# Optimization experiments

Hardware: AMD Instinct MI355X
Metric: run time of the kernel (lower is better)

Reference implementation:

```python
import jax, jax.numpy as jnp
import numpy as np

B, LQ, LK = 8, 1024, 1024
H, HD = 8, 128            # n_head, hidden_dim (per-head)
HEAD_DIM, CHILD_DIM = 512, 512
D_MODEL = HEAD_DIM + CHILD_DIM
TEMP = float(np.sqrt(HD))
NEG = 100000000.0
EPS = 1e-5


def setup_inputs() -> dict:
    key = jax.random.key(0)
    ks = jax.random.split(key, 12)
    q = jax.random.normal(ks[0], (B, LQ, HEAD_DIM), jnp.float32)
    k = jax.random.normal(ks[1], (B, LK, CHILD_DIM), jnp.float32)
    v = jax.random.normal(ks[2], (B, LK, D_MODEL), jnp.float32)
    old_score = 0.1 * jax.random.normal(ks[3], (H * B, LQ, LK), jnp.float32)
    float_mask = (jax.random.uniform(ks[4], (B, LQ, LK)) > 0.2).astype(jnp.float32)
    # torch nn.Linear weights are [out_features, in_features]
    wq = jax.random.normal(ks[5], (H * HD, HEAD_DIM), jnp.float32) * np.sqrt(2.0 / (HEAD_DIM + HD))
    wk = jax.random.normal(ks[6], (H * HD, CHILD_DIM), jnp.float32) * np.sqrt(2.0 / (CHILD_DIM + HD))
    wv = jax.random.normal(ks[7], (H * HD, D_MODEL), jnp.float32) * np.sqrt(2.0 / (D_MODEL + HD))
    wfc = jax.random.normal(ks[8], (D_MODEL, H * HD), jnp.float32) * np.sqrt(2.0 / (D_MODEL + H * HD))
    bq = jnp.zeros((H * HD,), jnp.float32)
    bk = jnp.zeros((H * HD,), jnp.float32)
    bv = jnp.zeros((H * HD,), jnp.float32)
    bfc = jnp.zeros((D_MODEL,), jnp.float32)
    ln_g = jnp.ones((D_MODEL,), jnp.float32)
    ln_b = jnp.zeros((D_MODEL,), jnp.float32)
    return dict(q=q, k=k, v=v, old_score=old_score, float_mask=float_mask,
                wq=wq, bq=bq, wk=wk, bk=bk, wv=wv, bv=bv,
                wfc=wfc, bfc=bfc, ln_g=ln_g, ln_b=ln_b)


def reference(q, k, v, old_score, float_mask, wq, bq, wk, bk, wv, bv, wfc, bfc, ln_g, ln_b):
    b, lq, _ = q.shape
    lk = k.shape[1]
    residual = v
    qh = (q @ wq.T + bq).reshape(b, lq, H, HD)   # [b,lq,h,d]
    kh = (k @ wk.T + bk).reshape(b, lk, H, HD)
    vh = (v @ wv.T + bv).reshape(b, lk, H, HD)
    # raw_score laid out head-major to match torch's (n_head*B, Lq, Lk)
    raw = jnp.einsum('bqhd,bkhd->hbqk', qh, kh) + old_score.reshape(H, b, lq, lk)
    score = raw - NEG * (1.0 - float_mask)[None]          # broadcast over heads
    attn = jax.nn.softmax(score / TEMP, axis=-1)          # eval path
    out = jnp.einsum('hbqk,bkhd->bqhd', attn, vh).reshape(b, lq, H * HD)
    out = out @ wfc.T + bfc + residual                    # dropout=identity (eval)
    mean = jnp.mean(out, axis=-1, keepdims=True)
    var = jnp.mean(jnp.square(out - mean), axis=-1, keepdims=True)
    out = (out - mean) / jnp.sqrt(var + EPS) * ln_g + ln_b
    return out, raw.reshape(H * b, lq, lk)
```

## Files before the change

### kernel.cpp

```cpp
#include <hip/hip_runtime.h>

typedef unsigned short u16;
typedef __bf16 bf16x8 __attribute__((ext_vector_type(8)));
typedef float f32x4 __attribute__((ext_vector_type(4)));

#define MFMA16(a,b,c) __builtin_amdgcn_mfma_f32_16x16x32_bf16(a,b,c,0,0,0)

static __device__ __forceinline__ u16 f2bf(float f){
  unsigned u = __builtin_bit_cast(unsigned, f);
  u += 0x7fffu + ((u>>16)&1u);
  return (u16)(u>>16);
}
static __device__ __forceinline__ int swz256(int r,int c){ return r*256 + (c ^ ((r&7)<<4)); }
static __device__ __forceinline__ int swz128(int r,int c){ return r*128 + (c ^ ((r&7)<<4)); }

static __device__ __forceinline__ void gload16(const void* g, void* l){
  __builtin_amdgcn_global_load_lds(
      (const __attribute__((address_space(1))) unsigned int*)g,
      (__attribute__((address_space(3))) unsigned int*)l, 16, 0, 0);
}

__global__ void conv_f2b(const float* __restrict__ in, u16* __restrict__ out, int n4){
  int i = blockIdx.x*256 + threadIdx.x;
  if (i >= n4) return;
  float4 f = reinterpret_cast<const float4*>(in)[i];
  ushort4 o; o.x=f2bf(f.x); o.y=f2bf(f.y); o.z=f2bf(f.z); o.w=f2bf(f.w);
  reinterpret_cast<ushort4*>(out)[i] = o;
}

template<int MODE>
__global__ __launch_bounds__(256) void gemm_nt(const u16* __restrict__ A, const u16* __restrict__ Bw,
    const float* __restrict__ bias, const float* __restrict__ resid,
    u16* __restrict__ Cb, float* __restrict__ Cf, int M, int N, int K)
{
  __shared__ uint4 ldsv[2048];
  char* la = (char*)ldsv;
  char* lb = la + 16384;
  const int tid = threadIdx.x, lane = tid&63, w = tid>>6;
  const int l15 = lane&15, l4 = lane>>4;
  const int wm = w&1, wn = w>>1;
  const int mb = blockIdx.x, nb = blockIdx.y;
  const f32x4 zero4 = {0.f,0.f,0.f,0.f};
  f32x4 acc[4][4];
  #pragma unroll
  for (int i=0;i<4;++i)
    #pragma unroll
    for (int j=0;j<4;++j) acc[i][j] = zero4;

  for (int k0=0;k0<K;k0+=64){
    __syncthreads();
    #pragma unroll
    for (int it=0; it<4; ++it){
      int slot = it*256 + tid;
      int r = slot>>3, cg = (slot&7) ^ (r&7);
      gload16(A + (size_t)(mb*128+r)*K + k0 + cg*8, la + (it*256 + w*64)*16);
      gload16(Bw + (size_t)(nb*128+r)*K + k0 + cg*8, lb + (it*256 + w*64)*16);
    }
    __syncthreads();
    #pragma unroll
    for (int kk=0;kk<2;++kk){
      bf16x8 af[4], bfr[4];
      #pragma unroll
      for (int i=0;i<4;++i){
        af[i]  = *reinterpret_cast<const bf16x8*>(la + swz128(wm*64+i*16+l15, (kk*32+l4*8)*2));
        bfr[i] = *reinterpret_cast<const bf16x8*>(lb + swz128(wn*64+i*16+l15, (kk*32+l4*8)*2));
      }
      #pragma unroll
      for (int i=0;i<4;++i)
        #pragma unroll
        for (int j=0;j<4;++j)
          acc[i][j] = MFMA16(af[i], bfr[j], acc[i][j]);
    }
  }
  #pragma unroll
  for (int j=0;j<4;++j){
    int col = nb*128 + wn*64 + j*16 + l15;
    float bv = bias[col];
    #pragma unroll
    for (int i=0;i<4;++i){
      int row0 = mb*128 + wm*64 + i*16 + l4*4;
      if (MODE == 0){
        #pragma unroll
        for (int r=0;r<4;++r)
          Cb[(size_t)(row0+r)*N + col] = f2bf(acc[i][j][r] + bv);
      } else if (MODE == 1){
        int bb = row0 >> 10, kp = row0 & 1023;
        ushort4 o;
        o.x = f2bf(acc[i][j][0]+bv); o.y = f2bf(acc[i][j][1]+bv);
        o.z = f2bf(acc[i][j][2]+bv); o.w = f2bf(acc[i][j][3]+bv);
        *reinterpret_cast<ushort4*>(Cb + (size_t)(bb*1024+col)*1024 + kp) = o;
      } else {
        #pragma unroll
        for (int r=0;r<4;++r){
          size_t off = (size_t)(row0+r)*N + col;
          Cf[off] = acc[i][j][r] + bv + resid[off];
        }
      }
    }
  }
}

__global__ __launch_bounds__(256) void attn_fused(const u16* __restrict__ qh,
    const u16* __restrict__ kh, const u16* __restrict__ vt,
    const float* __restrict__ oldsc, const float* __restrict__ fmask,
    float* __restrict__ raw, u16* __restrict__ ao)
{
  __shared__ uint4 ldsv[2560];
  char* lk_ = (char*)ldsv;
  char* lv_ = lk_ + 16384;
  char* lp_ = lk_ + 32768;
  const int tid = threadIdx.x, lane = tid&63, w = tid>>6;
  const int l15 = lane&15, l4 = lane>>4;
  const int qb = blockIdx.x, b = blockIdx.y, h = blockIdx.z;
  const float invT = 0.088388347648318447f;
  const f32x4 zero4 = {0.f,0.f,0.f,0.f};

  bf16x8 qf[4];
  {
    const u16* qp = qh + (size_t)(b*1024 + qb*64 + w*16 + l15)*1024 + h*128 + l4*8;
    #pragma unroll
    for (int kk=0;kk<4;++kk)
      qf[kk] = __builtin_bit_cast(bf16x8, *reinterpret_cast<const uint4*>(qp + kk*32));
  }
  f32x4 oacc[8];
  #pragma unroll
  for (int i=0;i<8;++i) oacc[i] = zero4;
  float mr[4], lr[4];
  #pragma unroll
  for (int r=0;r<4;++r){ mr[r] = -3.0e38f; lr[r] = 0.f; }

  const int qglob = qb*64 + w*16 + l4*4;

  for (int kt=0; kt<16; ++kt){
    __syncthreads();
    #pragma unroll
    for (int it=0; it<4; ++it){
      int slot = it*256 + tid;
      { int rs = slot>>4, cs = slot&15;
        int cg = cs ^ (rs&7);
        int kv = (rs&15)*4 + (rs>>4);
        gload16(kh + (size_t)(b*1024 + kt*64 + kv)*1024 + h*128 + cg*8,
                lk_ + (it*256 + w*64)*16); }
      { int r = slot>>3, cg = (slot&7) ^ (r&7);
        gload16(vt + (size_t)(b*1024 + h*128 + r)*1024 + kt*64 + cg*8,
                lv_ + (it*256 + w*64)*16); }
    }
    size_t rbase = ((size_t)(h*8 + b)*1024 + qglob)*1024 + kt*64 + l15*4;
    size_t mbase = ((size_t)b*1024 + qglob)*1024 + kt*64 + l15*4;
    float4 o4[4], m4[4];
    #pragma unroll
    for (int r=0;r<4;++r){
      o4[r] = *reinterpret_cast<const float4*>(oldsc + rbase + (size_t)r*1024);
      m4[r] = *reinterpret_cast<const float4*>(fmask + mbase + (size_t)r*1024);
    }
    __syncthreads();
    f32x4 fs[4];
    #pragma unroll
    for (int fj=0;fj<4;++fj){
      f32x4 s = zero4;
      #pragma unroll
      for (int kk=0;kk<4;++kk){
        bf16x8 kf = *reinterpret_cast<const bf16x8*>(lk_ + swz256(fj*16+l15, (kk*32+l4*8)*2));
        s = MFMA16(qf[kk], kf, s);
      }
      fs[fj] = s;
    }
    float tm[4];
    #pragma unroll
    for (int r=0;r<4;++r){
      float4 rv;
      rv.x = fs[0][r] + o4[r].x; rv.y = fs[1][r] + o4[r].y;
      rv.z = fs[2][r] + o4[r].z; rv.w = fs[3][r] + o4[r].w;
      *reinterpret_cast<float4*>(raw + rbase + (size_t)r*1024) = rv;
      fs[0][r] = (rv.x - 1.0e8f*(1.0f - m4[r].x)) * invT;
      fs[1][r] = (rv.y - 1.0e8f*(1.0f - m4[r].y)) * invT;
      fs[2][r] = (rv.z - 1.0e8f*(1.0f - m4[r].z)) * invT;
      fs[3][r] = (rv.w - 1.0e8f*(1.0f - m4[r].w)) * invT;
      tm[r] = fmaxf(fmaxf(fs[0][r], fs[1][r]), fmaxf(fs[2][r], fs[3][r]));
    }
    #pragma unroll
    for (int o=1;o<16;o<<=1){
      #pragma unroll
      for (int r=0;r<4;++r) tm[r] = fmaxf(tm[r], __shfl_xor(tm[r], o));
    }
    #pragma unroll
    for (int r=0;r<4;++r){
      float mn  = fmaxf(mr[r], tm[r]);
      float esc = __expf(mr[r] - mn);
      mr[r] = mn;
      lr[r] *= esc;
      #pragma unroll
      for (int nf=0;nf<8;++nf) oacc[nf][r] *= esc;
      float px = __expf(fs[0][r] - mn), py = __expf(fs[1][r] - mn);
      float pz = __expf(fs[2][r] - mn), pw = __expf(fs[3][r] - mn);
      lr[r] += px + py + pz + pw;
      ushort4 o;
      o.x = f2bf(px); o.y = f2bf(py); o.z = f2bf(pz); o.w = f2bf(pw);
      int prow = w*16 + l4*4 + r;
      *reinterpret_cast<ushort4*>(lp_ + swz128(prow, l15*8)) = o;
    }
    #pragma unroll
    for (int kkv=0;kkv<2;++kkv){
      bf16x8 pf = *reinterpret_cast<const bf16x8*>(lp_ + swz128(w*16+l15, (kkv*32+l4*8)*2));
      #pragma unroll
      for (int nf=0;nf<8;++nf){
        bf16x8 vf = *reinterpret_cast<const bf16x8*>(lv_ + swz128(nf*16+l15, (kkv*32+l4*8)*2));
        oacc[nf] = MFMA16(pf, vf, oacc[nf]);
      }
    }
  }
  #pragma unroll
  for (int o=1;o<16;o<<=1){
    #pragma unroll
    for (int r=0;r<4;++r) lr[r] += __shfl_xor(lr[r], o);
  }
  #pragma unroll
  for (int nf=0;nf<8;++nf){
    int col = h*128 + nf*16 + l15;
    #pragma unroll
    for (int r=0;r<4;++r){
      size_t orow = (size_t)(b*1024 + qb*64 + w*16 + l4*4 + r);
      ao[orow*1024 + col] = f2bf(oacc[nf][r] * (1.0f/lr[r]));
    }
  }
}

__global__ __launch_bounds__(256) void ln_k(float* __restrict__ io,
    const float* __restrict__ g, const float* __restrict__ bb)
{
  const int lane = threadIdx.x & 63, w = threadIdx.x >> 6;
  size_t row = (size_t)blockIdx.x*4 + w;
  float4* p = reinterpret_cast<float4*>(io + row*1024);
  float4 x[4];
  float s = 0.f, s2 = 0.f;
  #pragma unroll
  for (int i=0;i<4;++i){
    x[i] = p[lane + i*64];
    s  += x[i].x + x[i].y + x[i].z + x[i].w;
    s2 += x[i].x*x[i].x + x[i].y*x[i].y + x[i].z*x[i].z + x[i].w*x[i].w;
  }
  #pragma unroll
  for (int o=1;o<64;o<<=1){ s += __shfl_xor(s,o); s2 += __shfl_xor(s2,o); }
  float mean = s * 0.0009765625f;
  float var  = s2 * 0.0009765625f - mean*mean;
  float rstd = rsqrtf(var + 1e-5f);
  const float4* gp = reinterpret_cast<const float4*>(g);
  const float4* bp = reinterpret_cast<const float4*>(bb);
  #pragma unroll
  for (int i=0;i<4;++i){
    float4 gg = gp[lane+i*64], bv = bp[lane+i*64], y;
    y.x = (x[i].x-mean)*rstd*gg.x + bv.x;
    y.y = (x[i].y-mean)*rstd*gg.y + bv.y;
    y.z = (x[i].z-mean)*rstd*gg.z + bv.z;
    y.w = (x[i].w-mean)*rstd*gg.w + bv.w;
    p[lane+i*64] = y;
  }
}

extern "C" void kernel_launch(void* const* d_in, const int* in_sizes, int n_in,
                              void* d_out, int out_size, void* d_ws, size_t ws_size,
                              hipStream_t stream)
{
  const float* q    = (const float*)d_in[0];
  const float* k    = (const float*)d_in[1];
  const float* v    = (const float*)d_in[2];
  const float* olds = (const float*)d_in[3];
  const float* fm   = (const float*)d_in[4];
  const float* wq   = (const float*)d_in[5];
  const float* bq   = (const float*)d_in[6];
  const float* wk   = (const float*)d_in[7];
  const float* bk   = (const float*)d_in[8];
  const float* wv   = (const float*)d_in[9];
  const float* bv   = (const float*)d_in[10];
  const float* wfc  = (const float*)d_in[11];
  const float* bfc  = (const float*)d_in[12];
  const float* lng  = (const float*)d_in[13];
  const float* lnb  = (const float*)d_in[14];
  float* out = (float*)d_out;
  float* raw = out + 8388608;

  u16* ws  = (u16*)d_ws;
  u16* qbf = ws;
  u16* kbf = qbf + 4194304;
  u16* vbf = kbf + 4194304;
  u16* wqb = vbf + 8388608;
  u16* wkb = wqb + 524288;
  u16* wvb = wkb + 524288;
  u16* wfb = wvb + 1048576;
  u16* qhb = wfb + 1048576;
  u16* khb = qhb + 8388608;
  u16* vtb = khb + 8388608;
  u16* aob = vtb + 8388608;

  conv_f2b<<<4096,256,0,stream>>>(q,   qbf, 1048576);
  conv_f2b<<<4096,256,0,stream>>>(k,   kbf, 1048576);
  conv_f2b<<<8192,256,0,stream>>>(v,   vbf, 2097152);
  conv_f2b<<<512, 256,0,stream>>>(wq,  wqb, 131072);
  conv_f2b<<<512, 256,0,stream>>>(wk,  wkb, 131072);
  conv_f2b<<<1024,256,0,stream>>>(wv,  wvb, 262144);
  conv_f2b<<<1024,256,0,stream>>>(wfc, wfb, 262144);

  gemm_nt<0><<<dim3(64,8),256,0,stream>>>(qbf, wqb, bq, nullptr, qhb, nullptr, 8192,1024,512);
  gemm_nt<0><<<dim3(64,8),256,0,stream>>>(kbf, wkb, bk, nullptr, khb, nullptr, 8192,1024,512);
  gemm_nt<1><<<dim3(64,8),256,0,stream>>>(vbf, wvb, bv, nullptr, vtb, nullptr, 8192,1024,1024);

  attn_fused<<<dim3(16,8,8),256,0,stream>>>(qhb, khb, vtb, olds, fm, raw, aob);

  gemm_nt<2><<<dim3(64,8),256,0,stream>>>(aob, wfb, bfc, v, nullptr, out, 8192,1024,1024);
  ln_k<<<2048,256,0,stream>>>(out, lng, lnb);
}
```

Measured before the change: 316.1 us.

## Double-buffer K/V tiles and prefetch old_score/mask in attention kernel

Splits the attention loop into stage, prefetch and compute steps and ping-pongs between two LDS buffers for the K and V tiles. The next tile's K/V global-to-LDS loads and old_score/mask register loads are issued before the current tile is computed, so memory latency can overlap the MFMA work and one barrier per iteration is removed. In exchange, LDS use per block nearly doubles, which lowers the number of resident blocks per CU. The barrier at the end of each body step may also force all outstanding loads to finish, which would limit how much overlap is actually achieved.

```diff
diff --git a/kernel.cpp b/kernel.cpp
--- a/kernel.cpp
+++ b/kernel.cpp
@@ -105,16 +105,25 @@
     const float* __restrict__ oldsc, const float* __restrict__ fmask,
     float* __restrict__ raw, u16* __restrict__ ao)
 {
-  __shared__ uint4 ldsv[2560];
-  char* lk_ = (char*)ldsv;
-  char* lv_ = lk_ + 16384;
-  char* lp_ = lk_ + 32768;
+  __shared__ uint4 ldsv[4608];
+  char* lk0 = (char*)ldsv;
+  char* lv0 = lk0 + 16384;
+  char* lk1 = lk0 + 32768;
+  char* lv1 = lk0 + 49152;
+  char* lp_ = lk0 + 65536;
   const int tid = threadIdx.x, lane = tid&63, w = tid>>6;
   const int l15 = lane&15, l4 = lane>>4;
   const int qb = blockIdx.x, b = blockIdx.y, h = blockIdx.z;
   const float invT = 0.088388347648318447f;
   const f32x4 zero4 = {0.f,0.f,0.f,0.f};
 
+  const int qglob = qb*64 + w*16 + l4*4;
+  const float* oldp = oldsc + ((size_t)(h*8+b)*1024 + qglob)*1024 + l15*4;
+  const float* fmp  = fmask + ((size_t)b*1024 + qglob)*1024 + l15*4;
+  float*       rawp = raw   + ((size_t)(h*8+b)*1024 + qglob)*1024 + l15*4;
+  const u16* khB = kh + (size_t)b*1024*1024 + h*128;
+  const u16* vtB = vt + ((size_t)b*1024 + h*128)*1024;
+
   bf16x8 qf[4];
   {
     const u16* qp = qh + (size_t)(b*1024 + qb*64 + w*16 + l15)*1024 + h*128 + l4*8;
@@ -129,38 +138,33 @@
   #pragma unroll
   for (int r=0;r<4;++r){ mr[r] = -3.0e38f; lr[r] = 0.f; }
 
-  const int qglob = qb*64 + w*16 + l4*4;
-
-  for (int kt=0; kt<16; ++kt){
-    __syncthreads();
+  auto stage = [&](int kt, char* lkD, char* lvD){
     #pragma unroll
     for (int it=0; it<4; ++it){
       int slot = it*256 + tid;
-      { int rs = slot>>4, cs = slot&15;
-        int cg = cs ^ (rs&7);
-        int kv = (rs&15)*4 + (rs>>4);
-        gload16(kh + (size_t)(b*1024 + kt*64 + kv)*1024 + h*128 + cg*8,
-                lk_ + (it*256 + w*64)*16); }
-      { int r = slot>>3, cg = (slot&7) ^ (r&7);
-        gload16(vt + (size_t)(b*1024 + h*128 + r)*1024 + kt*64 + cg*8,
-                lv_ + (it*256 + w*64)*16); }
-    }
-    size_t rbase = ((size_t)(h*8 + b)*1024 + qglob)*1024 + kt*64 + l15*4;
-    size_t mbase = ((size_t)b*1024 + qglob)*1024 + kt*64 + l15*4;
-    float4 o4[4], m4[4];
+      int rs = slot>>4, cs = slot&15;
+      int cgk = cs ^ (rs&7);
+      int kv = (rs&15)*4 + (rs>>4);
+      gload16(khB + (size_t)(kt*64 + kv)*1024 + cgk*8, lkD + (it*256 + w*64)*16);
+      int r8 = slot>>3, cgv = (slot&7) ^ (r8&7);
+      gload16(vtB + (size_t)r8*1024 + kt*64 + cgv*8, lvD + (it*256 + w*64)*16);
+    }
+  };
+  auto pref = [&](int kt, float4 (&o4)[4], float4 (&m4)[4]){
     #pragma unroll
     for (int r=0;r<4;++r){
-      o4[r] = *reinterpret_cast<const float4*>(oldsc + rbase + (size_t)r*1024);
-      m4[r] = *reinterpret_cast<const float4*>(fmask + mbase + (size_t)r*1024);
-    }
-    __syncthreads();
+      o4[r] = *reinterpret_cast<const float4*>(oldp + (size_t)r*1024 + kt*64);
+      m4[r] = *reinterpret_cast<const float4*>(fmp  + (size_t)r*1024 + kt*64);
+    }
+  };
+  auto body = [&](int kt, char* lkR, char* lvR, float4 (&o4)[4], float4 (&m4)[4]){
     f32x4 fs[4];
     #pragma unroll
     for (int fj=0;fj<4;++fj){
       f32x4 s = zero4;
       #pragma unroll
       for (int kk=0;kk<4;++kk){
-        bf16x8 kf = *reinterpret_cast<const bf16x8*>(lk_ + swz256(fj*16+l15, (kk*32+l4*8)*2));
+        bf16x8 kf = *reinterpret_cast<const bf16x8*>(lkR + swz256(fj*16+l15, (kk*32+l4*8)*2));
         s = MFMA16(qf[kk], kf, s);
       }
       fs[fj] = s;
@@ -171,7 +175,7 @@
       float4 rv;
       rv.x = fs[0][r] + o4[r].x; rv.y = fs[1][r] + o4[r].y;
       rv.z = fs[2][r] + o4[r].z; rv.w = fs[3][r] + o4[r].w;
-      *reinterpret_cast<float4*>(raw + rbase + (size_t)r*1024) = rv;
+      *reinterpret_cast<float4*>(rawp + (size_t)r*1024 + kt*64) = rv;
       fs[0][r] = (rv.x - 1.0e8f*(1.0f - m4[r].x)) * invT;
       fs[1][r] = (rv.y - 1.0e8f*(1.0f - m4[r].y)) * invT;
       fs[2][r] = (rv.z - 1.0e8f*(1.0f - m4[r].z)) * invT;
@@ -204,11 +208,25 @@
       bf16x8 pf = *reinterpret_cast<const bf16x8*>(lp_ + swz128(w*16+l15, (kkv*32+l4*8)*2));
       #pragma unroll
       for (int nf=0;nf<8;++nf){
-        bf16x8 vf = *reinterpret_cast<const bf16x8*>(lv_ + swz128(nf*16+l15, (kkv*32+l4*8)*2));
+        bf16x8 vf = *reinterpret_cast<const bf16x8*>(lvR + swz128(nf*16+l15, (kkv*32+l4*8)*2));
         oacc[nf] = MFMA16(pf, vf, oacc[nf]);
       }
     }
-  }
+    __syncthreads();
+  };
+
+  float4 oA[4], mA[4], oB[4], mB[4];
+  stage(0, lk0, lv0);
+  pref(0, oA, mA);
+  __syncthreads();
+  for (int kt=0; kt<16; kt+=2){
+    stage(kt+1, lk1, lv1);
+    pref(kt+1, oB, mB);
+    body(kt, lk0, lv0, oA, mA);
+    if (kt+2 < 16){ stage(kt+2, lk0, lv0); pref(kt+2, oA, mA); }
+    body(kt+1, lk1, lv1, oB, mB);
+  }
+
   #pragma unroll
   for (int o=1;o<16;o<<=1){
     #pragma unroll
```

New measurement: 313.2 us. About the same (-0.9%).

## Bitpack mask, widen attention KV tile, prefetch old_score, remap blocks to XCDs

Applied to the files above, without the earlier changes.

Packs the float mask into one bit per element in a pre-pass, so the attention kernel reads 1/32 of the mask bytes it read before. The attention kernel now uses 128-wide KV tiles (LDS doubled) and prefetches old_score and mask bits one tile ahead, with double-buffered registers and explicit waitcnt/barrier scheduling. It also remaps the 1D grid so that blocks sharing the same (b,h) K/V land on the same XCD for L2 reuse. The cost is an extra kernel launch plus more LDS and registers, which can lower occupancy.

```diff
diff --git a/kernel.cpp b/kernel.cpp
--- a/kernel.cpp
+++ b/kernel.cpp
@@ -26,6 +26,22 @@
   float4 f = reinterpret_cast<const float4*>(in)[i];
   ushort4 o; o.x=f2bf(f.x); o.y=f2bf(f.y); o.z=f2bf(f.z); o.w=f2bf(f.w);
   reinterpret_cast<ushort4*>(out)[i] = o;
+}
+
+__global__ void mask2bits(const float* __restrict__ fm, unsigned char* __restrict__ bits){
+  int i = blockIdx.x*256 + threadIdx.x;
+  const float4* p = reinterpret_cast<const float4*>(fm + (size_t)i*8);
+  float4 a = p[0], bq = p[1];
+  unsigned v = 0;
+  v |= (a.x  > 0.5f) ? 1u   : 0u;
+  v |= (a.y  > 0.5f) ? 2u   : 0u;
+  v |= (a.z  > 0.5f) ? 4u   : 0u;
+  v |= (a.w  > 0.5f) ? 8u   : 0u;
+  v |= (bq.x > 0.5f) ? 16u  : 0u;
+  v |= (bq.y > 0.5f) ? 32u  : 0u;
+  v |= (bq.z > 0.5f) ? 64u  : 0u;
+  v |= (bq.w > 0.5f) ? 128u : 0u;
+  bits[i] = (unsigned char)v;
 }
 
 template<int MODE>
@@ -102,18 +118,28 @@
 
 __global__ __launch_bounds__(256) void attn_fused(const u16* __restrict__ qh,
     const u16* __restrict__ kh, const u16* __restrict__ vt,
-    const float* __restrict__ oldsc, const float* __restrict__ fmask,
+    const float* __restrict__ oldsc, const unsigned char* __restrict__ bits,
     float* __restrict__ raw, u16* __restrict__ ao)
 {
-  __shared__ uint4 ldsv[2560];
+  __shared__ uint4 ldsv[5120];
   char* lk_ = (char*)ldsv;
-  char* lv_ = lk_ + 16384;
-  char* lp_ = lk_ + 32768;
+  char* lv_ = lk_ + 32768;
+  char* lp_ = lk_ + 65536;
   const int tid = threadIdx.x, lane = tid&63, w = tid>>6;
   const int l15 = lane&15, l4 = lane>>4;
-  const int qb = blockIdx.x, b = blockIdx.y, h = blockIdx.z;
+  unsigned u = blockIdx.x;
+  int slotid = (u & 7) * 128 + (u >> 3);
+  const int qb = slotid & 15, bh = slotid >> 4;
+  const int b = bh & 7, h = bh >> 3;
   const float invT = 0.088388347648318447f;
   const f32x4 zero4 = {0.f,0.f,0.f,0.f};
+
+  const int qglob = qb*64 + w*16 + l4*4;
+  const float* oldp = oldsc + ((size_t)(h*8+b)*1024 + qglob)*1024 + l15*8;
+  float*       rawp = raw   + ((size_t)(h*8+b)*1024 + qglob)*1024 + l15*8;
+  const unsigned char* bitp = bits + ((size_t)b*1024 + qglob)*128 + l15;
+  const u16* khB = kh + (size_t)b*1024*1024 + h*128;
+  const u16* vtB = vt + ((size_t)b*1024 + h*128)*1024;
 
   bf16x8 qf[4];
   {
@@ -129,34 +155,35 @@
   #pragma unroll
   for (int r=0;r<4;++r){ mr[r] = -3.0e38f; lr[r] = 0.f; }
 
-  const int qglob = qb*64 + w*16 + l4*4;
-
-  for (int kt=0; kt<16; ++kt){
-    __syncthreads();
-    #pragma unroll
-    for (int it=0; it<4; ++it){
+  auto stage = [&](int kt){
+    #pragma unroll
+    for (int it=0; it<8; ++it){
       int slot = it*256 + tid;
-      { int rs = slot>>4, cs = slot&15;
-        int cg = cs ^ (rs&7);
-        int kv = (rs&15)*4 + (rs>>4);
-        gload16(kh + (size_t)(b*1024 + kt*64 + kv)*1024 + h*128 + cg*8,
-                lk_ + (it*256 + w*64)*16); }
-      { int r = slot>>3, cg = (slot&7) ^ (r&7);
-        gload16(vt + (size_t)(b*1024 + h*128 + r)*1024 + kt*64 + cg*8,
-                lv_ + (it*256 + w*64)*16); }
-    }
-    size_t rbase = ((size_t)(h*8 + b)*1024 + qglob)*1024 + kt*64 + l15*4;
-    size_t mbase = ((size_t)b*1024 + qglob)*1024 + kt*64 + l15*4;
-    float4 o4[4], m4[4];
+      int rs = slot>>4, cs = slot&15;
+      int ck = cs ^ (rs&7);
+      int ks = (rs&15)*8 + (rs>>4);
+      gload16(khB + (size_t)(kt*128 + ks)*1024 + ck*8, lk_ + (it*256 + w*64)*16);
+    }
+    #pragma unroll
+    for (int it=0; it<8; ++it){
+      int slot = it*256 + tid;
+      int rs = slot>>4, cs = slot&15;
+      int cv = cs ^ (rs&7);
+      gload16(vtB + (size_t)rs*1024 + kt*128 + cv*8, lv_ + (it*256 + w*64)*16);
+    }
+  };
+  auto pref = [&](int kt, float4 (&o8)[4][2], unsigned (&bb)[4]){
     #pragma unroll
     for (int r=0;r<4;++r){
-      o4[r] = *reinterpret_cast<const float4*>(oldsc + rbase + (size_t)r*1024);
-      m4[r] = *reinterpret_cast<const float4*>(fmask + mbase + (size_t)r*1024);
-    }
-    __syncthreads();
-    f32x4 fs[4];
-    #pragma unroll
-    for (int fj=0;fj<4;++fj){
+      o8[r][0] = *reinterpret_cast<const float4*>(oldp + (size_t)r*1024 + kt*128);
+      o8[r][1] = *reinterpret_cast<const float4*>(oldp + (size_t)r*1024 + kt*128 + 4);
+      bb[r] = bitp[(size_t)r*128 + kt*16];
+    }
+  };
+  auto body = [&](int kt, float4 (&o8)[4][2], unsigned (&bb)[4]){
+    f32x4 fs[8];
+    #pragma unroll
+    for (int fj=0;fj<8;++fj){
       f32x4 s = zero4;
       #pragma unroll
       for (int kk=0;kk<4;++kk){
@@ -168,15 +195,25 @@
     float tm[4];
     #pragma unroll
     for (int r=0;r<4;++r){
-      float4 rv;
-      rv.x = fs[0][r] + o4[r].x; rv.y = fs[1][r] + o4[r].y;
-      rv.z = fs[2][r] + o4[r].z; rv.w = fs[3][r] + o4[r].w;
-      *reinterpret_cast<float4*>(raw + rbase + (size_t)r*1024) = rv;
-      fs[0][r] = (rv.x - 1.0e8f*(1.0f - m4[r].x)) * invT;
-      fs[1][r] = (rv.y - 1.0e8f*(1.0f - m4[r].y)) * invT;
-      fs[2][r] = (rv.z - 1.0e8f*(1.0f - m4[r].z)) * invT;
-      fs[3][r] = (rv.w - 1.0e8f*(1.0f - m4[r].w)) * invT;
-      tm[r] = fmaxf(fmaxf(fs[0][r], fs[1][r]), fmaxf(fs[2][r], fs[3][r]));
+      float4 r0, r1;
+      r0.x = fs[0][r] + o8[r][0].x; r0.y = fs[1][r] + o8[r][0].y;
+      r0.z = fs[2][r] + o8[r][0].z; r0.w = fs[3][r] + o8[r][0].w;
+      r1.x = fs[4][r] + o8[r][1].x; r1.y = fs[5][r] + o8[r][1].y;
+      r1.z = fs[6][r] + o8[r][1].z; r1.w = fs[7][r] + o8[r][1].w;
+      float4* rp = reinterpret_cast<float4*>(rawp + (size_t)r*1024 + kt*128);
+      rp[0] = r0; rp[1] = r1;
+      unsigned bv = bb[r];
+      fs[0][r] = (r0.x - ((bv&1u)  ? 0.f : 1.0e8f)) * invT;
+      fs[1][r] = (r0.y - ((bv&2u)  ? 0.f : 1.0e8f)) * invT;
+      fs[2][r] = (r0.z - ((bv&4u)  ? 0.f : 1.0e8f)) * invT;
+      fs[3][r] = (r0.w - ((bv&8u)  ? 0.f : 1.0e8f)) * invT;
+      fs[4][r] = (r1.x - ((bv&16u) ? 0.f : 1.0e8f)) * invT;
+      fs[5][r] = (r1.y - ((bv&32u) ? 0.f : 1.0e8f)) * invT;
+      fs[6][r] = (r1.z - ((bv&64u) ? 0.f : 1.0e8f)) * invT;
+      fs[7][r] = (r1.w - ((bv&128u)? 0.f : 1.0e8f)) * invT;
+      float m0 = fmaxf(fmaxf(fs[0][r],fs[1][r]), fmaxf(fs[2][r],fs[3][r]));
+      float m1 = fmaxf(fmaxf(fs[4][r],fs[5][r]), fmaxf(fs[6][r],fs[7][r]));
+      tm[r] = fmaxf(m0, m1);
     }
     #pragma unroll
     for (int o=1;o<16;o<<=1){
@@ -191,24 +228,56 @@
       lr[r] *= esc;
       #pragma unroll
       for (int nf=0;nf<8;++nf) oacc[nf][r] *= esc;
-      float px = __expf(fs[0][r] - mn), py = __expf(fs[1][r] - mn);
-      float pz = __expf(fs[2][r] - mn), pw = __expf(fs[3][r] - mn);
-      lr[r] += px + py + pz + pw;
-      ushort4 o;
-      o.x = f2bf(px); o.y = f2bf(py); o.z = f2bf(pz); o.w = f2bf(pw);
+      float p[8];
+      float ls = 0.f;
+      #pragma unroll
+      for (int fj=0;fj<8;++fj){ p[fj] = __expf(fs[fj][r] - mn); ls += p[fj]; }
+      lr[r] += ls;
+      u16 pk[8];
+      #pragma unroll
+      for (int fj=0;fj<8;++fj) pk[fj] = f2bf(p[fj]);
       int prow = w*16 + l4*4 + r;
-      *reinterpret_cast<ushort4*>(lp_ + swz128(prow, l15*8)) = o;
-    }
-    #pragma unroll
-    for (int kkv=0;kkv<2;++kkv){
-      bf16x8 pf = *reinterpret_cast<const bf16x8*>(lp_ + swz128(w*16+l15, (kkv*32+l4*8)*2));
+      *reinterpret_cast<uint4*>(lp_ + swz256(prow, l15*16)) =
+          *reinterpret_cast<const uint4*>(pk);
+    }
+    #pragma unroll
+    for (int kkv=0;kkv<4;++kkv){
+      bf16x8 pf = *reinterpret_cast<const bf16x8*>(lp_ + swz256(w*16+l15, (kkv*32+l4*8)*2));
       #pragma unroll
       for (int nf=0;nf<8;++nf){
-        bf16x8 vf = *reinterpret_cast<const bf16x8*>(lv_ + swz128(nf*16+l15, (kkv*32+l4*8)*2));
+        bf16x8 vf = *reinterpret_cast<const bf16x8*>(lv_ + swz256(nf*16+l15, (kkv*32+l4*8)*2));
         oacc[nf] = MFMA16(pf, vf, oacc[nf]);
       }
     }
-  }
+  };
+
+  float4 oA[4][2], oB[4][2];
+  unsigned bA[4], bB[4];
+  pref(0, oA, bA);
+  #pragma unroll 1
+  for (int kt=0; kt<8; kt+=2){
+    __builtin_amdgcn_s_barrier();
+    stage(kt);
+    __builtin_amdgcn_sched_barrier(0);
+    pref(kt+1, oB, bB);
+    __builtin_amdgcn_sched_barrier(0);
+    asm volatile("s_waitcnt vmcnt(12)" ::: "memory");
+    __builtin_amdgcn_sched_barrier(0);
+    __builtin_amdgcn_s_barrier();
+    __builtin_amdgcn_sched_barrier(0);
+    body(kt, oA, bA);
+    __builtin_amdgcn_s_barrier();
+    stage(kt+1);
+    __builtin_amdgcn_sched_barrier(0);
+    pref(kt+2 < 8 ? kt+2 : 7, oA, bA);
+    __builtin_amdgcn_sched_barrier(0);
+    asm volatile("s_waitcnt vmcnt(12)" ::: "memory");
+    __builtin_amdgcn_sched_barrier(0);
+    __builtin_amdgcn_s_barrier();
+    __builtin_amdgcn_sched_barrier(0);
+    body(kt+1, oB, bB);
+  }
+
   #pragma unroll
   for (int o=1;o<16;o<<=1){
     #pragma unroll
@@ -291,6 +360,7 @@
   u16* khb = qhb + 8388608;
   u16* vtb = khb + 8388608;
   u16* aob = vtb + 8388608;
+  unsigned char* bits = (unsigned char*)(aob + 8388608);
 
   conv_f2b<<<4096,256,0,stream>>>(q,   qbf, 1048576);
   conv_f2b<<<4096,256,0,stream>>>(k,   kbf, 1048576);
@@ -299,12 +369,13 @@
   conv_f2b<<<512, 256,0,stream>>>(wk,  wkb, 131072);
   conv_f2b<<<1024,256,0,stream>>>(wv,  wvb, 262144);
   conv_f2b<<<1024,256,0,stream>>>(wfc, wfb, 262144);
+  mask2bits<<<4096,256,0,stream>>>(fm, bits);
 
   gemm_nt<0><<<dim3(64,8),256,0,stream>>>(qbf, wqb, bq, nullptr, qhb, nullptr, 8192,1024,512);
   gemm_nt<0><<<dim3(64,8),256,0,stream>>>(kbf, wkb, bk, nullptr, khb, nullptr, 8192,1024,512);
   gemm_nt<1><<<dim3(64,8),256,0,stream>>>(vbf, wvb, bv, nullptr, vtb, nullptr, 8192,1024,1024);
 
-  attn_fused<<<dim3(16,8,8),256,0,stream>>>(qhb, khb, vtb, olds, fm, raw, aob);
+  attn_fused<<<1024,256,0,stream>>>(qhb, khb, vtb, olds, bits, raw, aob);
 
   gemm_nt<2><<<dim3(64,8),256,0,stream>>>(aob, wfb, bfc, v, nullptr, out, 8192,1024,1024);
   ln_k<<<2048,256,0,stream>>>(out, lng, lnb);
```

Result: slower. 354.2 us (+12.0%).
